# Performance work log

Measured on AMD Instinct MI355X. Metric: run time of the kernel, lower is better.

## Reference

```python
import jax, jax.numpy as jnp
import numpy as np

HIDDEN = 4096
HEADS = 32
HEAD_DIM = HIDDEN // HEADS  # 128; kv length must equal this (additive-bias broadcast)
B, SQ, SK = 4, 2048, HEAD_DIM


def _split_heads(x):
    # [B, T, HIDDEN] -> [B, H, T, d]
    b, t, _ = x.shape
    return x.reshape(b, t, HEADS, HEAD_DIM).transpose(0, 2, 1, 3)


def setup_inputs() -> dict:
    key = jax.random.key(0)
    ks = jax.random.split(key, 8)
    s = 1.0 / np.sqrt(HIDDEN)
    return {
        "q": jax.random.normal(ks[0], (B, SQ, HIDDEN), jnp.float32),
        "k": jax.random.normal(ks[1], (B, SK, HIDDEN), jnp.float32),
        "v": jax.random.normal(ks[2], (B, SK, HIDDEN), jnp.float32),
        "r": jax.random.normal(ks[3], (B, SQ, HIDDEN), jnp.float32),
        "Wq": jax.random.normal(ks[4], (HIDDEN, HIDDEN), jnp.float32) * s,
        "Wk": jax.random.normal(ks[5], (HIDDEN, HIDDEN), jnp.float32) * s,
        "Wv": jax.random.normal(ks[6], (HIDDEN, HIDDEN), jnp.float32) * s,
        "Wo": jax.random.normal(ks[7], (HIDDEN, HIDDEN), jnp.float32) * s,
    }


def reference(q, k, v, r, Wq, Wk, Wv, Wo):
    qh = _split_heads(q @ Wq)           # [B,H,SQ,d]
    kh = _split_heads(k @ Wk)           # [B,H,SK,d]
    vh = _split_heads(v @ Wv)           # [B,H,SK,d]
    rh = _split_heads(r @ Wo)           # [B,H,SQ,d] ; d == SK, added as bias
    scale = 1.0 / np.sqrt(HEAD_DIM).astype(np.float32)
    scores = jnp.einsum("bhqd,bhkd->bhqk", qh, kh) * scale + rh
    attn = jax.nn.softmax(scores, axis=-1)
    ctx = jnp.einsum("bhqk,bhkd->bhqd", attn, vh)       # [B,H,SQ,d]
    ctx = ctx.transpose(0, 2, 1, 3).reshape(q.shape[0], -1, HIDDEN)
    return ctx @ Wo  # Wo reused for output projection, as in source
```

## Files before the change

kernel.cpp:

```cpp
#include <hip/hip_runtime.h>
#include <hip/hip_bf16.h>

typedef unsigned short u16;
typedef unsigned int   u32;
typedef unsigned long long u64;
typedef __attribute__((ext_vector_type(8))) short short8;
typedef __attribute__((ext_vector_type(4))) float f32x4;

#define HID   4096
#define NHEAD 32
#define HD    128
#define NB    4
#define NSQ   2048
#define NSK   128
#define MROWS (NB*NSQ)
#define KROWS (NB*NSK)

__device__ __forceinline__ u16 f2bf(float f) {
  u32 u = __builtin_bit_cast(u32, f);
  u += 0x7fffu + ((u >> 16) & 1u);
  return (u16)(u >> 16);
}

__device__ __forceinline__ u64 pack4(float4 f) {
  return (u64)f2bf(f.x) | ((u64)f2bf(f.y) << 16) |
         ((u64)f2bf(f.z) << 32) | ((u64)f2bf(f.w) << 48);
}

__device__ __forceinline__ uint4 packu16x8(const u16* v) {
  uint4 o;
  o.x = (u32)v[0] | ((u32)v[1] << 16);
  o.y = (u32)v[2] | ((u32)v[3] << 16);
  o.z = (u32)v[4] | ((u32)v[5] << 16);
  o.w = (u32)v[6] | ((u32)v[7] << 16);
  return o;
}

__device__ __forceinline__ f32x4 mfma16(short8 a, short8 b, f32x4 c) {
  return __builtin_amdgcn_mfma_f32_16x16x32_bf16(a, b, c, 0, 0, 0);
}

__device__ __forceinline__ void gload_lds16(const u16* g, u16* l) {
  __builtin_amdgcn_global_load_lds((const __attribute__((address_space(1))) u32*)g,
                                   (__attribute__((address_space(3))) u32*)l, 16, 0, 0);
}

__global__ __launch_bounds__(256) void convert_bf16(const float* __restrict__ in,
                                                    u16* __restrict__ out, long long n4)
{
  long long i = (long long)blockIdx.x * blockDim.x + threadIdx.x;
  const long long stride = (long long)gridDim.x * blockDim.x;
  for (; i < n4; i += stride) {
    float4 f = ((const float4*)in)[i];
    ((u64*)out)[i] = pack4(f);
  }
}

__global__ __launch_bounds__(256) void convert_bf16_x2(const float* __restrict__ in0,
                                                       u16* __restrict__ out0,
                                                       const float* __restrict__ in1,
                                                       u16* __restrict__ out1, long long n4)
{
  const float* in = blockIdx.y ? in1 : in0;
  u16* out = blockIdx.y ? out1 : out0;
  long long i = (long long)blockIdx.x * blockDim.x + threadIdx.x;
  const long long stride = (long long)gridDim.x * blockDim.x;
  for (; i < n4; i += stride) {
    float4 f = ((const float4*)in)[i];
    ((u64*)out)[i] = pack4(f);
  }
}

__global__ __launch_bounds__(256) void transpose_convert_x2(const float* __restrict__ W0,
                                                            u16* __restrict__ T0,
                                                            const float* __restrict__ W1,
                                                            u16* __restrict__ T1)
{
  const float* W = blockIdx.z ? W1 : W0;
  u16* Wt = blockIdx.z ? T1 : T0;
  __shared__ __align__(16) u16 tile[64][72];
  const int t = threadIdx.x;
  const int c0 = blockIdx.x * 64, r0 = blockIdx.y * 64;
  #pragma unroll
  for (int i = 0; i < 4; ++i) {
    int e = i * 1024 + t * 4;
    int rr = e >> 6, cc = e & 63;
    float4 f = *(const float4*)(W + (size_t)(r0 + rr) * HID + c0 + cc);
    *(u64*)&tile[rr][cc] = pack4(f);
  }
  __syncthreads();
  #pragma unroll
  for (int i = 0; i < 2; ++i) {
    int e = i * 2048 + t * 8;
    int cc = e >> 6, rr = e & 63;
    u16 vals[8];
    #pragma unroll
    for (int jj = 0; jj < 8; ++jj) vals[jj] = tile[rr + jj][cc];
    *(uint4*)(Wt + (size_t)(c0 + cc) * HID + r0 + rr) = packu16x8(vals);
  }
}

__global__ __launch_bounds__(256) void transpose_head(const u16* __restrict__ Vh,
                                                      u16* __restrict__ VT)
{
  __shared__ __align__(16) u16 tile[128][136];
  const int t = threadIdx.x;
  const int bh = blockIdx.x;
  const int b = bh >> 5, h = bh & 31;
  #pragma unroll
  for (int i = 0; i < 8; ++i) {
    int e = i * 2048 + t * 8;
    int tr = e >> 7, d = e & 127;
    *(uint4*)&tile[tr][d] = *(const uint4*)(Vh + ((size_t)b * NSK + tr) * HID + h * HD + d);
  }
  __syncthreads();
  #pragma unroll
  for (int i = 0; i < 8; ++i) {
    int e = i * 2048 + t * 8;
    int d = e >> 7, tt = e & 127;
    u16 vals[8];
    #pragma unroll
    for (int jj = 0; jj < 8; ++jj) vals[jj] = tile[tt + jj][d];
    *(uint4*)(VT + ((size_t)bh * HD + d) * NSK + tt) = packu16x8(vals);
  }
}


__device__ __forceinline__ short8 ldf(const u16* buf, int r, int cb) {
  return *(const short8*)(buf + r * 64 + (cb ^ ((r & 7) << 3)));
}

__device__ __forceinline__ void stage2(u16* dst, const u16* g, long off0, long off1, int tid) {
  gload_lds16(g + off0, dst + tid * 8);
  gload_lds16(g + off1, dst + 4096 + tid * 8);
}

#define BAR() do { __builtin_amdgcn_sched_barrier(0); __builtin_amdgcn_s_barrier(); \
                   __builtin_amdgcn_sched_barrier(0); } while (0)

#define MFMA8(R0, C0, AV, BV) do { \
  __builtin_amdgcn_s_setprio(1); \
  _Pragma("unroll") \
  for (int _i = 0; _i < 4; ++_i) { \
    acc[(R0) + _i][(C0)]     = mfma16(AV[_i], BV[0], acc[(R0) + _i][(C0)]); \
    acc[(R0) + _i][(C0) + 1] = mfma16(AV[_i], BV[1], acc[(R0) + _i][(C0) + 1]); \
  } \
  __builtin_amdgcn_s_setprio(0); \
} while (0)

template<int VM7, int VM8, bool S1, bool S2, bool NEXT>
__device__ __forceinline__ void tile8(const u16* __restrict__ Ag, const u16* __restrict__ Bg,
                                      int kt, u16* Ac, u16* Bc, u16* Ao, u16* Bo,
                                      int wm, int wn, int g8, int c16,
                                      long off0, long off1, int tid,
                                      short8 (&aA)[4], short8 (&aB)[4],
                                      short8 (&bLa)[2], short8 (&bLb)[2], short8 (&bB)[2],
                                      f32x4 (&acc)[8][4])
{
  #pragma unroll
  for (int j = 0; j < 2; ++j) bB[j] = ldf(Bc, wn * 64 + (2 + j) * 16 + c16, g8);
  if constexpr (S1) stage2(Ao + 8192, Ag + (size_t)128 * HID + kt + 64, off0, off1, tid);
  BAR();
  MFMA8(0, 0, aA, bLa);
  #pragma unroll
  for (int i = 0; i < 4; ++i) aB[i] = ldf(Ac, wm * 128 + 64 + i * 16 + c16, g8);
  if constexpr (S1) stage2(Bo + 8192, Bg + (size_t)128 * HID + kt + 64, off0, off1, tid);
  BAR();
  MFMA8(0, 2, aA, bB);
  BAR();
  MFMA8(4, 2, aB, bB);
  #pragma unroll
  for (int i = 0; i < 4; ++i) aA[i] = ldf(Ac, wm * 128 + i * 16 + c16, 32 + g8);
  #pragma unroll
  for (int j = 0; j < 2; ++j) bLb[j] = ldf(Bc, wn * 64 + j * 16 + c16, 32 + g8);
  BAR();
  MFMA8(4, 0, aB, bLa);
  #pragma unroll
  for (int j = 0; j < 2; ++j) bB[j] = ldf(Bc, wn * 64 + (2 + j) * 16 + c16, 32 + g8);
  BAR();
  MFMA8(0, 0, aA, bLb);
  #pragma unroll
  for (int i = 0; i < 4; ++i) aB[i] = ldf(Ac, wm * 128 + 64 + i * 16 + c16, 32 + g8);
  BAR();
  MFMA8(0, 2, aA, bB);
  if constexpr (S2) stage2(Bc, Bg + kt + 128, off0, off1, tid);
  if constexpr (VM7 >= 0) asm volatile("s_waitcnt vmcnt(%0)" :: "n"(VM7) : "memory");
  BAR();
  MFMA8(4, 2, aB, bB);
  if constexpr (NEXT) {
    #pragma unroll
    for (int i = 0; i < 4; ++i) aA[i] = ldf(Ao, wm * 128 + i * 16 + c16, g8);
    #pragma unroll
    for (int j = 0; j < 2; ++j) bLa[j] = ldf(Bo, wn * 64 + j * 16 + c16, g8);
  }
  if constexpr (S2) stage2(Ac, Ag + kt + 128, off0, off1, tid);
  if constexpr (VM8 >= 0) asm volatile("s_waitcnt vmcnt(%0)" :: "n"(VM8) : "memory");
  BAR();
  MFMA8(4, 0, aB, bLb);
}

template<bool OUTF32, bool EXTRA>
__global__ __launch_bounds__(512, 2) void gemm256(const u16* __restrict__ A,
                                                  const u16* __restrict__ Bt,
                                                  void* __restrict__ Cv,
                                                  const u16* __restrict__ A2,
                                                  const u16* __restrict__ BtK,
                                                  const u16* __restrict__ BtV,
                                                  u16* __restrict__ KhO,
                                                  u16* __restrict__ VhO)
{
  __shared__ __align__(16) u16 As[2][16384];
  __shared__ __align__(16) u16 Bs[2][16384];
  const int tid = threadIdx.x;
  const int l = tid & 63, wv = tid >> 6;
  const int g8 = (l >> 4 & 3) * 8, c16 = l & 15;
  const int g = l >> 4 & 3;
  const int wm = wv >> 2, wn = wv & 3;

  const int nwg = gridDim.x;
  int wg = blockIdx.x;
  wg = (wg & 7) * (nwg >> 3) + (wg >> 3);

  const u16* Ag; const u16* Bg; u16* Ch = nullptr; float* Cf = nullptr; int n0;
  if constexpr (EXTRA) {
    if (wg >= 512) {
      const int e = wg - 512, mt = e >> 4;
      n0 = (e & 15) * 256;
      Ag = A2 + (size_t)(mt << 8) * HID;
      Bg = (mt < 2 ? BtK : BtV) + (size_t)n0 * HID;
      Ch = (mt < 2 ? KhO : VhO) + (size_t)((mt & 1) << 8) * HID;
    } else {
      const int m0 = (wg >> 4) * 256; n0 = (wg & 15) * 256;
      Ag = A + (size_t)m0 * HID;
      Bg = Bt + (size_t)n0 * HID;
      Ch = (u16*)Cv + (size_t)m0 * HID;
    }
  } else {
    const int m0 = (wg >> 4) * 256; n0 = (wg & 15) * 256;
    Ag = A + (size_t)m0 * HID;
    Bg = Bt + (size_t)n0 * HID;
    if constexpr (OUTF32) Cf = (float*)Cv + (size_t)m0 * HID;
    else                  Ch = (u16*)Cv + (size_t)m0 * HID;
  }

  const long off0 = (long)(tid >> 3) * HID + (((tid & 7) ^ ((tid >> 3) & 7)) * 8);
  const long off1 = off0 + (long)64 * HID;

  f32x4 acc[8][4] = {};
  short8 aA[4], aB[4], bLa[2], bLb[2], bB[2];

  stage2(&Bs[0][0],    Bg,                     off0, off1, tid);
  stage2(&As[0][0],    Ag,                     off0, off1, tid);
  stage2(&As[0][8192], Ag + (size_t)128 * HID, off0, off1, tid);
  stage2(&Bs[0][8192], Bg + (size_t)128 * HID, off0, off1, tid);
  stage2(&Bs[1][0],    Bg + 64,                off0, off1, tid);
  stage2(&As[1][0],    Ag + 64,                off0, off1, tid);
  asm volatile("s_waitcnt vmcnt(4)" ::: "memory");
  BAR();
  #pragma unroll
  for (int i = 0; i < 4; ++i) aA[i] = ldf(&As[0][0], wm * 128 + i * 16 + c16, g8);
  #pragma unroll
  for (int j = 0; j < 2; ++j) bLa[j] = ldf(&Bs[0][0], wn * 64 + j * 16 + c16, g8);

  constexpr int NT = HID / 64;
  for (int T = 0; T < NT - 2; T += 2) {
    tile8<6, 4, true, true, true>(Ag, Bg, T * 64,      &As[0][0], &Bs[0][0], &As[1][0], &Bs[1][0],
                                  wm, wn, g8, c16, off0, off1, tid, aA, aB, bLa, bLb, bB, acc);
    tile8<6, 4, true, true, true>(Ag, Bg, T * 64 + 64, &As[1][0], &Bs[1][0], &As[0][0], &Bs[0][0],
                                  wm, wn, g8, c16, off0, off1, tid, aA, aB, bLa, bLb, bB, acc);
  }
  tile8<4, 0, true, false, true>(Ag, Bg, (NT - 2) * 64, &As[0][0], &Bs[0][0], &As[1][0], &Bs[1][0],
                                 wm, wn, g8, c16, off0, off1, tid, aA, aB, bLa, bLb, bB, acc);
  tile8<-1, -1, false, false, false>(Ag, Bg, (NT - 1) * 64, &As[1][0], &Bs[1][0], &As[0][0], &Bs[0][0],
                                     wm, wn, g8, c16, off0, off1, tid, aA, aB, bLa, bLb, bB, acc);

  #pragma unroll
  for (int mi = 0; mi < 8; ++mi)
    #pragma unroll
    for (int j = 0; j < 4; ++j)
      #pragma unroll
      for (int rr = 0; rr < 4; ++rr) {
        const size_t idx = (size_t)(wm * 128 + mi * 16 + g * 4 + rr) * HID
                         + n0 + wn * 64 + j * 16 + c16;
        if constexpr (OUTF32) Cf[idx] = acc[mi][j][rr];
        else                  Ch[idx] = f2bf(acc[mi][j][rr]);
      }
}

__global__ __launch_bounds__(256) void attn_kernel(const u16*  __restrict__ Qh,
                                                   const u16*  __restrict__ Kh,
                                                   const u16*  __restrict__ VT,
                                                   const float* __restrict__ Rh,
                                                   u16* __restrict__ ctx)
{
  __shared__ __align__(16) u16 Plds[4][32][136];
  const int t = threadIdx.x;
  const int w = t >> 6, l = t & 63;
  const int g = l >> 4, c = l & 15;
  const int qc = blockIdx.x;
  const int bh = blockIdx.y;
  const int b = bh >> 5, h = bh & 31;
  const size_t qrow0 = (size_t)b * NSQ + qc * 128 + w * 32;
  const float SCALE = 0.08838834764831845f;

  f32x4 s[2][8] = {};
  #pragma unroll
  for (int ks = 0; ks < 4; ++ks) {
    const int ko = ks * 32 + g * 8;
    short8 af[2];
    #pragma unroll
    for (int i = 0; i < 2; ++i)
      af[i] = *(const short8*)(Qh + (qrow0 + i * 16 + c) * HID + h * HD + ko);
    #pragma unroll
    for (int j = 0; j < 8; ++j) {
      short8 bfr = *(const short8*)(Kh + ((size_t)b * NSK + j * 16 + c) * HID + h * HD + ko);
      s[0][j] = mfma16(af[0], bfr, s[0][j]);
      s[1][j] = mfma16(af[1], bfr, s[1][j]);
    }
  }

  float rinv[2][4];
  #pragma unroll
  for (int i = 0; i < 2; ++i) {
    #pragma unroll
    for (int rr = 0; rr < 4; ++rr) {
      const size_t qr = qrow0 + i * 16 + g * 4 + rr;
      float vmax = -3.0e38f;
      #pragma unroll
      for (int j = 0; j < 8; ++j) {
        float bias = Rh[qr * HID + h * HD + j * 16 + c];
        float sv = s[i][j][rr] * SCALE + bias;
        s[i][j][rr] = sv;
        vmax = fmaxf(vmax, sv);
      }
      #pragma unroll
      for (int m = 1; m < 16; m <<= 1) vmax = fmaxf(vmax, __shfl_xor(vmax, m));
      float ssum = 0.f;
      #pragma unroll
      for (int j = 0; j < 8; ++j) {
        float p = __expf(s[i][j][rr] - vmax);
        s[i][j][rr] = p;
        ssum += p;
      }
      #pragma unroll
      for (int m = 1; m < 16; m <<= 1) ssum += __shfl_xor(ssum, m);
      rinv[i][rr] = 1.f / ssum;
    }
  }

  #pragma unroll
  for (int i = 0; i < 2; ++i)
    #pragma unroll
    for (int j = 0; j < 8; ++j)
      #pragma unroll
      for (int rr = 0; rr < 4; ++rr)
        Plds[w][i * 16 + g * 4 + rr][j * 16 + c] = f2bf(s[i][j][rr]);
  __syncthreads();

  #pragma unroll
  for (int i = 0; i < 2; ++i) {
    f32x4 o[8] = {};
    #pragma unroll
    for (int ks = 0; ks < 4; ++ks) {
      const int ko = ks * 32 + g * 8;
      short8 pa = *(const short8*)(&Plds[w][i * 16 + c][ko]);
      #pragma unroll
      for (int j = 0; j < 8; ++j) {
        short8 bv = *(const short8*)(VT + ((size_t)bh * HD + j * 16 + c) * NSK + ko);
        o[j] = mfma16(pa, bv, o[j]);
      }
    }
    #pragma unroll
    for (int j = 0; j < 8; ++j)
      #pragma unroll
      for (int rr = 0; rr < 4; ++rr) {
        const size_t row = qrow0 + i * 16 + g * 4 + rr;
        ctx[row * HID + h * HD + j * 16 + c] = f2bf(o[j][rr] * rinv[i][rr]);
      }
  }
}

extern "C" void kernel_launch(void* const* d_in, const int* in_sizes, int n_in,
                              void* d_out, int out_size, void* d_ws, size_t ws_size,
                              hipStream_t stream)
{
  const float* q  = (const float*)d_in[0];
  const float* k  = (const float*)d_in[1];
  const float* v  = (const float*)d_in[2];
  const float* r  = (const float*)d_in[3];
  const float* Wq = (const float*)d_in[4];
  const float* Wk = (const float*)d_in[5];
  const float* Wv = (const float*)d_in[6];
  const float* Wo = (const float*)d_in[7];
  float* out = (float*)d_out;

  char* ws = (char*)d_ws;
  #define WSMB(x) ((size_t)(x) << 20)
  u16* WoT = (u16*)(ws + WSMB(0));
  u16* Qh  = (u16*)(ws + WSMB(32));
  u16* Kh  = (u16*)(ws + WSMB(96));
  u16* Vh  = (u16*)(ws + WSMB(100));
  u16* VTb = (u16*)(ws + WSMB(104));
  u16* ctx = (u16*)(ws + WSMB(108));
  u16* kb  = (u16*)(ws + WSMB(108));
  u16* vb  = (u16*)(ws + WSMB(112));
  u16* Sb  = (u16*)(ws + WSMB(172));
  u16* WqT = (u16*)(ws + WSMB(236));
  u16* WkT = (u16*)((char*)d_out + WSMB(0));
  u16* WvT = (u16*)((char*)d_out + WSMB(32));
  const size_t needed = WSMB(268);
  if (ws_size < needed) return;

  dim3 tb(256);
  dim3 tb5(512);
  const long long nBig = (long long)MROWS * HID / 4;
  const long long nSm  = (long long)KROWS * HID / 4;

  transpose_convert_x2<<<dim3(64, 64, 2), tb, 0, stream>>>(Wo, WoT, Wq, WqT);
  transpose_convert_x2<<<dim3(64, 64, 2), tb, 0, stream>>>(Wk, WkT, Wv, WvT);
  convert_bf16_x2<<<dim3(512, 2), tb, 0, stream>>>(k, kb, v, vb, nSm);
  convert_bf16<<<dim3(2048), tb, 0, stream>>>(q, Sb, nBig);

  gemm256<false, true><<<dim3(576), tb5, 0, stream>>>(Sb, WqT, (void*)Qh,
                                                      kb, WkT, WvT, Kh, Vh);

  convert_bf16<<<dim3(2048), tb, 0, stream>>>(r, Sb, nBig);
  gemm256<true, false><<<dim3(512), tb5, 0, stream>>>(Sb, WoT, (void*)out,
                                                      nullptr, nullptr, nullptr, nullptr, nullptr);

  transpose_head<<<dim3(128), tb, 0, stream>>>(Vh, VTb);

  attn_kernel<<<dim3(16, 128), tb, 0, stream>>>(Qh, Kh, VTb, out, ctx);

  gemm256<true, false><<<dim3(512), tb5, 0, stream>>>(ctx, WoT, (void*)out,
                                                      nullptr, nullptr, nullptr, nullptr, nullptr);
}
```

Measured before the change: 1.209 ms.

## Restructure GEMM inner pipeline to 4 phases and batch conversion launches

The GEMM main loop now runs four phases per k-tile, each issuing 16 MFMAs from a 4x4 fragment set, instead of eight phases of 8 MFMAs. This halves the barriers per tile and changes how LDS fragment loads and global-to-LDS staging interleave with compute, at the cost of more fragment registers. Separately, the four weight transpose-converts are merged into one launch, and the q and r fp32-to-bf16 conversions are merged into one launch. To make room for this, k/v bf16 buffers move into the output buffer and r gets its own workspace slot.

```diff
diff --git a/kernel.cpp b/kernel.cpp
--- a/kernel.cpp
+++ b/kernel.cpp
@@ -45,17 +45,6 @@
                                    (__attribute__((address_space(3))) u32*)l, 16, 0, 0);
 }
 
-__global__ __launch_bounds__(256) void convert_bf16(const float* __restrict__ in,
-                                                    u16* __restrict__ out, long long n4)
-{
-  long long i = (long long)blockIdx.x * blockDim.x + threadIdx.x;
-  const long long stride = (long long)gridDim.x * blockDim.x;
-  for (; i < n4; i += stride) {
-    float4 f = ((const float4*)in)[i];
-    ((u64*)out)[i] = pack4(f);
-  }
-}
-
 __global__ __launch_bounds__(256) void convert_bf16_x2(const float* __restrict__ in0,
                                                        u16* __restrict__ out0,
                                                        const float* __restrict__ in1,
@@ -71,13 +60,14 @@
   }
 }
 
-__global__ __launch_bounds__(256) void transpose_convert_x2(const float* __restrict__ W0,
-                                                            u16* __restrict__ T0,
-                                                            const float* __restrict__ W1,
-                                                            u16* __restrict__ T1)
-{
-  const float* W = blockIdx.z ? W1 : W0;
-  u16* Wt = blockIdx.z ? T1 : T0;
+__global__ __launch_bounds__(256) void transpose_convert_x4(const float* __restrict__ W0, u16* __restrict__ T0,
+                                                            const float* __restrict__ W1, u16* __restrict__ T1,
+                                                            const float* __restrict__ W2, u16* __restrict__ T2,
+                                                            const float* __restrict__ W3, u16* __restrict__ T3)
+{
+  const int z = blockIdx.z;
+  const float* W = (z == 0) ? W0 : (z == 1) ? W1 : (z == 2) ? W2 : W3;
+  u16* Wt = (z == 0) ? T0 : (z == 1) ? T1 : (z == 2) ? T2 : T3;
   __shared__ __align__(16) u16 tile[64][72];
   const int t = threadIdx.x;
   const int c0 = blockIdx.x * 64, r0 = blockIdx.y * 64;
@@ -138,65 +128,55 @@
 #define BAR() do { __builtin_amdgcn_sched_barrier(0); __builtin_amdgcn_s_barrier(); \
                    __builtin_amdgcn_sched_barrier(0); } while (0)
 
-#define MFMA8(R0, C0, AV, BV) do { \
+#define MFMA16(R0, AV, BV) do { \
   __builtin_amdgcn_s_setprio(1); \
   _Pragma("unroll") \
-  for (int _i = 0; _i < 4; ++_i) { \
-    acc[(R0) + _i][(C0)]     = mfma16(AV[_i], BV[0], acc[(R0) + _i][(C0)]); \
-    acc[(R0) + _i][(C0) + 1] = mfma16(AV[_i], BV[1], acc[(R0) + _i][(C0) + 1]); \
-  } \
+  for (int _i = 0; _i < 4; ++_i) \
+    _Pragma("unroll") \
+    for (int _j = 0; _j < 4; ++_j) \
+      acc[(R0) + _i][_j] = mfma16(AV[_i], BV[_j], acc[(R0) + _i][_j]); \
   __builtin_amdgcn_s_setprio(0); \
 } while (0)
 
-template<int VM7, int VM8, bool S1, bool S2, bool NEXT>
-__device__ __forceinline__ void tile8(const u16* __restrict__ Ag, const u16* __restrict__ Bg,
-                                      int kt, u16* Ac, u16* Bc, u16* Ao, u16* Bo,
-                                      int wm, int wn, int g8, int c16,
-                                      long off0, long off1, int tid,
-                                      short8 (&aA)[4], short8 (&aB)[4],
-                                      short8 (&bLa)[2], short8 (&bLb)[2], short8 (&bB)[2],
-                                      f32x4 (&acc)[8][4])
-{
-  #pragma unroll
-  for (int j = 0; j < 2; ++j) bB[j] = ldf(Bc, wn * 64 + (2 + j) * 16 + c16, g8);
+template<int VM, bool S1, bool S2, bool NEXT>
+__device__ __forceinline__ void tile4p(const u16* __restrict__ Ag, const u16* __restrict__ Bg,
+                                       int kt, u16* Ac, u16* Bc, u16* Ao, u16* Bo,
+                                       int wm, int wn, int g8, int c16,
+                                       long off0, long off1, int tid,
+                                       short8 (&afA)[4], short8 (&afB)[4],
+                                       short8 (&bfA)[4], short8 (&bfB)[4],
+                                       f32x4 (&acc)[8][4])
+{
+  #pragma unroll
+  for (int i = 0; i < 4; ++i) afB[i] = ldf(Ac, wm * 128 + 64 + i * 16 + c16, g8);
   if constexpr (S1) stage2(Ao + 8192, Ag + (size_t)128 * HID + kt + 64, off0, off1, tid);
   BAR();
-  MFMA8(0, 0, aA, bLa);
-  #pragma unroll
-  for (int i = 0; i < 4; ++i) aB[i] = ldf(Ac, wm * 128 + 64 + i * 16 + c16, g8);
+  MFMA16(0, afA, bfA);
+
+  #pragma unroll
+  for (int i = 0; i < 4; ++i) afA[i] = ldf(Ac, wm * 128 + i * 16 + c16, 32 + g8);
+  #pragma unroll
+  for (int j = 0; j < 4; ++j) bfB[j] = ldf(Bc, wn * 64 + j * 16 + c16, 32 + g8);
   if constexpr (S1) stage2(Bo + 8192, Bg + (size_t)128 * HID + kt + 64, off0, off1, tid);
   BAR();
-  MFMA8(0, 2, aA, bB);
+  MFMA16(4, afB, bfA);
+
+  #pragma unroll
+  for (int i = 0; i < 4; ++i) afB[i] = ldf(Ac, wm * 128 + 64 + i * 16 + c16, 32 + g8);
+  if constexpr (S2) stage2(Bc, Bg + kt + 128, off0, off1, tid);
   BAR();
-  MFMA8(4, 2, aB, bB);
-  #pragma unroll
-  for (int i = 0; i < 4; ++i) aA[i] = ldf(Ac, wm * 128 + i * 16 + c16, 32 + g8);
-  #pragma unroll
-  for (int j = 0; j < 2; ++j) bLb[j] = ldf(Bc, wn * 64 + j * 16 + c16, 32 + g8);
+  MFMA16(0, afA, bfB);
+
+  if constexpr (S2) stage2(Ac, Ag + kt + 128, off0, off1, tid);
+  if constexpr (VM >= 0) asm volatile("s_waitcnt vmcnt(%0)" :: "n"(VM) : "memory");
   BAR();
-  MFMA8(4, 0, aB, bLa);
-  #pragma unroll
-  for (int j = 0; j < 2; ++j) bB[j] = ldf(Bc, wn * 64 + (2 + j) * 16 + c16, 32 + g8);
-  BAR();
-  MFMA8(0, 0, aA, bLb);
-  #pragma unroll
-  for (int i = 0; i < 4; ++i) aB[i] = ldf(Ac, wm * 128 + 64 + i * 16 + c16, 32 + g8);
-  BAR();
-  MFMA8(0, 2, aA, bB);
-  if constexpr (S2) stage2(Bc, Bg + kt + 128, off0, off1, tid);
-  if constexpr (VM7 >= 0) asm volatile("s_waitcnt vmcnt(%0)" :: "n"(VM7) : "memory");
-  BAR();
-  MFMA8(4, 2, aB, bB);
   if constexpr (NEXT) {
     #pragma unroll
-    for (int i = 0; i < 4; ++i) aA[i] = ldf(Ao, wm * 128 + i * 16 + c16, g8);
-    #pragma unroll
-    for (int j = 0; j < 2; ++j) bLa[j] = ldf(Bo, wn * 64 + j * 16 + c16, g8);
-  }
-  if constexpr (S2) stage2(Ac, Ag + kt + 128, off0, off1, tid);
-  if constexpr (VM8 >= 0) asm volatile("s_waitcnt vmcnt(%0)" :: "n"(VM8) : "memory");
-  BAR();
-  MFMA8(4, 0, aB, bLb);
+    for (int i = 0; i < 4; ++i) afA[i] = ldf(Ao, wm * 128 + i * 16 + c16, g8);
+    #pragma unroll
+    for (int j = 0; j < 4; ++j) bfA[j] = ldf(Bo, wn * 64 + j * 16 + c16, g8);
+  }
+  MFMA16(4, afB, bfB);
 }
 
 template<bool OUTF32, bool EXTRA>
@@ -247,7 +227,7 @@
   const long off1 = off0 + (long)64 * HID;
 
   f32x4 acc[8][4] = {};
-  short8 aA[4], aB[4], bLa[2], bLb[2], bB[2];
+  short8 afA[4], afB[4], bfA[4], bfB[4];
 
   stage2(&Bs[0][0],    Bg,                     off0, off1, tid);
   stage2(&As[0][0],    Ag,                     off0, off1, tid);
@@ -258,21 +238,21 @@
   asm volatile("s_waitcnt vmcnt(4)" ::: "memory");
   BAR();
   #pragma unroll
-  for (int i = 0; i < 4; ++i) aA[i] = ldf(&As[0][0], wm * 128 + i * 16 + c16, g8);
-  #pragma unroll
-  for (int j = 0; j < 2; ++j) bLa[j] = ldf(&Bs[0][0], wn * 64 + j * 16 + c16, g8);
+  for (int i = 0; i < 4; ++i) afA[i] = ldf(&As[0][0], wm * 128 + i * 16 + c16, g8);
+  #pragma unroll
+  for (int j = 0; j < 4; ++j) bfA[j] = ldf(&Bs[0][0], wn * 64 + j * 16 + c16, g8);
 
   constexpr int NT = HID / 64;
   for (int T = 0; T < NT - 2; T += 2) {
-    tile8<6, 4, true, true, true>(Ag, Bg, T * 64,      &As[0][0], &Bs[0][0], &As[1][0], &Bs[1][0],
-                                  wm, wn, g8, c16, off0, off1, tid, aA, aB, bLa, bLb, bB, acc);
-    tile8<6, 4, true, true, true>(Ag, Bg, T * 64 + 64, &As[1][0], &Bs[1][0], &As[0][0], &Bs[0][0],
-                                  wm, wn, g8, c16, off0, off1, tid, aA, aB, bLa, bLb, bB, acc);
-  }
-  tile8<4, 0, true, false, true>(Ag, Bg, (NT - 2) * 64, &As[0][0], &Bs[0][0], &As[1][0], &Bs[1][0],
-                                 wm, wn, g8, c16, off0, off1, tid, aA, aB, bLa, bLb, bB, acc);
-  tile8<-1, -1, false, false, false>(Ag, Bg, (NT - 1) * 64, &As[1][0], &Bs[1][0], &As[0][0], &Bs[0][0],
-                                     wm, wn, g8, c16, off0, off1, tid, aA, aB, bLa, bLb, bB, acc);
+    tile4p<4, true, true, true>(Ag, Bg, T * 64,      &As[0][0], &Bs[0][0], &As[1][0], &Bs[1][0],
+                                wm, wn, g8, c16, off0, off1, tid, afA, afB, bfA, bfB, acc);
+    tile4p<4, true, true, true>(Ag, Bg, T * 64 + 64, &As[1][0], &Bs[1][0], &As[0][0], &Bs[0][0],
+                                wm, wn, g8, c16, off0, off1, tid, afA, afB, bfA, bfB, acc);
+  }
+  tile4p<0, true, false, true>(Ag, Bg, (NT - 2) * 64, &As[0][0], &Bs[0][0], &As[1][0], &Bs[1][0],
+                               wm, wn, g8, c16, off0, off1, tid, afA, afB, bfA, bfB, acc);
+  tile4p<-1, false, false, false>(Ag, Bg, (NT - 1) * 64, &As[1][0], &Bs[1][0], &As[0][0], &Bs[0][0],
+                                  wm, wn, g8, c16, off0, off1, tid, afA, afB, bfA, bfB, acc);
 
   #pragma unroll
   for (int mi = 0; mi < 8; ++mi)
@@ -401,13 +381,14 @@
   u16* Kh  = (u16*)(ws + WSMB(96));
   u16* Vh  = (u16*)(ws + WSMB(100));
   u16* VTb = (u16*)(ws + WSMB(104));
+  u16* rb  = (u16*)(ws + WSMB(108));
   u16* ctx = (u16*)(ws + WSMB(108));
-  u16* kb  = (u16*)(ws + WSMB(108));
-  u16* vb  = (u16*)(ws + WSMB(112));
   u16* Sb  = (u16*)(ws + WSMB(172));
   u16* WqT = (u16*)(ws + WSMB(236));
   u16* WkT = (u16*)((char*)d_out + WSMB(0));
   u16* WvT = (u16*)((char*)d_out + WSMB(32));
+  u16* kb  = (u16*)((char*)d_out + WSMB(64));
+  u16* vb  = (u16*)((char*)d_out + WSMB(68));
   const size_t needed = WSMB(268);
   if (ws_size < needed) return;
 
@@ -416,16 +397,14 @@
   const long long nBig = (long long)MROWS * HID / 4;
   const long long nSm  = (long long)KROWS * HID / 4;
 
-  transpose_convert_x2<<<dim3(64, 64, 2), tb, 0, stream>>>(Wo, WoT, Wq, WqT);
-  transpose_convert_x2<<<dim3(64, 64, 2), tb, 0, stream>>>(Wk, WkT, Wv, WvT);
+  transpose_convert_x4<<<dim3(64, 64, 4), tb, 0, stream>>>(Wo, WoT, Wq, WqT, Wk, WkT, Wv, WvT);
   convert_bf16_x2<<<dim3(512, 2), tb, 0, stream>>>(k, kb, v, vb, nSm);
-  convert_bf16<<<dim3(2048), tb, 0, stream>>>(q, Sb, nBig);
+  convert_bf16_x2<<<dim3(2048, 2), tb, 0, stream>>>(q, Sb, r, rb, nBig);
 
   gemm256<false, true><<<dim3(576), tb5, 0, stream>>>(Sb, WqT, (void*)Qh,
                                                       kb, WkT, WvT, Kh, Vh);
 
-  convert_bf16<<<dim3(2048), tb, 0, stream>>>(r, Sb, nBig);
-  gemm256<true, false><<<dim3(512), tb5, 0, stream>>>(Sb, WoT, (void*)out,
+  gemm256<true, false><<<dim3(512), tb5, 0, stream>>>(rb, WoT, (void*)out,
                                                       nullptr, nullptr, nullptr, nullptr, nullptr);
 
   transpose_head<<<dim3(128), tb, 0, stream>>>(Vh, VTb);
```

New measurement: 1.175 ms. 1.03x faster.
